# Kernel tuning notes

Hardware: AMD Instinct MI355X
Metric: run time of the kernel (lower is better)

Reference implementation:

```python
import jax, jax.numpy as jnp
import numpy as np

P = 7            # roi_align_size
S = 2            # sampling grid per bin (mmcv sampling_ratio fixed to 2 for static shapes)
CAV = (-140.8, -40.0, -3.0, 140.8, 40.0, 1.0)
ENLARGE = 1.0

def _bilinear(fmap, b, x, y):
    # fmap: [B,H,W,C]; b,x,y: [N,P,P,S,S]; returns [N,P,P,S,S,C]
    H, W = fmap.shape[1], fmap.shape[2]
    valid = (y > -1.0) & (y < H) & (x > -1.0) & (x < W)
    y = jnp.maximum(y, 0.0)
    x = jnp.maximum(x, 0.0)
    y0 = jnp.minimum(jnp.floor(y).astype(jnp.int32), H - 1)
    x0 = jnp.minimum(jnp.floor(x).astype(jnp.int32), W - 1)
    y1 = jnp.minimum(y0 + 1, H - 1)
    x1 = jnp.minimum(x0 + 1, W - 1)
    # mmcv: if low index is at the border, snap the coordinate onto it
    yf = jnp.where(y0 >= H - 1, y0.astype(y.dtype), y)
    xf = jnp.where(x0 >= W - 1, x0.astype(x.dtype), x)
    ly = yf - y0.astype(y.dtype); lx = xf - x0.astype(x.dtype)
    hy = 1.0 - ly; hx = 1.0 - lx
    v00 = fmap[b, y0, x0]; v01 = fmap[b, y0, x1]
    v10 = fmap[b, y1, x0]; v11 = fmap[b, y1, x1]
    out = ((hy * hx)[..., None] * v00 + (hy * lx)[..., None] * v01
           + (ly * hx)[..., None] * v10 + (ly * lx)[..., None] * v11)
    return out * valid.astype(out.dtype)[..., None]

def _forward(feature, boxes, mask):
    B, C, H, W = feature.shape
    M = boxes.shape[1]
    gw = (CAV[3] - CAV[0]) / W
    gh = (CAV[4] - CAV[1]) / H
    flat = boxes.reshape(B * M, 7)  # mask is all ones -> every box is a roi
    b_idx = jnp.repeat(jnp.arange(B, dtype=jnp.int32), M)
    # roi in grid coords; spatial_scale=1, aligned=True (center offset -0.5)
    cx = (flat[:, 0] - CAV[0]) / gw - 0.5
    cy = (flat[:, 1] - CAV[1]) / gh - 0.5
    rw = flat[:, 5] / gw * ENLARGE
    rh = flat[:, 4] / gh * ENLARGE
    theta = -flat[:, 6]             # clockwise=True -> negate angle
    bin_w = rw / P; bin_h = rh / P
    pw = jnp.arange(P, dtype=feature.dtype)
    sw = (jnp.arange(S, dtype=feature.dtype) + 0.5) / S
    # per-roi local sample coords: [N,P,S]
    xx = (-rw / 2.0)[:, None, None] + bin_w[:, None, None] * (pw[None, :, None] + sw[None, None, :])
    yy = (-rh / 2.0)[:, None, None] + bin_h[:, None, None] * (pw[None, :, None] + sw[None, None, :])
    cosv = jnp.cos(theta)[:, None, None, None, None]
    sinv = jnp.sin(theta)[:, None, None, None, None]
    Y = yy[:, :, None, :, None]     # [N,ph,1,iy,1]
    X = xx[:, None, :, None, :]     # [N,1,pw,1,ix]
    ys = Y * cosv - X * sinv + cy[:, None, None, None, None]
    xs = Y * sinv + X * cosv + cx[:, None, None, None, None]
    fmap = jnp.transpose(feature, (0, 2, 3, 1))   # [B,H,W,C] for channel-last gathers
    b = jnp.broadcast_to(b_idx[:, None, None, None, None], ys.shape)
    vals = _bilinear(fmap, b, xs, ys)             # [N,P,P,S,S,C]
    pooled = vals.mean(axis=(3, 4))               # [N,P,P,C] == torch .permute(0,2,3,1)
    return pooled

def setup_inputs():
    key = jax.random.key(0)
    k1, k2 = jax.random.split(key, 2)
    B, C, H, W, M = 4, 256, 256, 256, 100
    feature = jax.random.normal(k1, (B, C, H, W), jnp.float32)
    u = jax.random.uniform(k2, (B, M, 7), jnp.float32)
    boxes = jnp.stack([
        u[..., 0] * 200.0 - 100.0,       # x center in [-100,100] m
        u[..., 1] * 60.0 - 30.0,         # y center in [-30,30] m
        u[..., 2] * 2.0 - 1.0,           # z (unused)
        u[..., 3] * 2.0 + 1.0,           # dim (unused)
        u[..., 4] * 2.0 + 1.5,           # extent mapped to H axis
        u[..., 5] * 3.0 + 2.0,           # extent mapped to W axis
        u[..., 6] * 2.0 * np.pi - np.pi, # yaw
    ], axis=-1)
    mask = jnp.ones((B, M), jnp.float32)
    return {"feature": feature, "object_bbx_center": boxes, "object_bbx_mask": mask}

def reference(feature, object_bbx_center, object_bbx_mask):
    return _forward(feature, object_bbx_center, object_bbx_mask)
```

## Files before the change

kernel.cpp:

```cpp
#include <hip/hip_runtime.h>


#define RP 7
#define RS 2
#define RGN 16
#define CG 32
#define CSTRIDE (RGN * RGN + 1)
#define NSAMP (RP * RP * RS * RS)

__global__ __launch_bounds__(256) void roialign_kernel(
    const float* __restrict__ feature,
    const float* __restrict__ boxes,
    float* __restrict__ out,
    int C, int H, int W, int M)
{
    __shared__ float  sm[CG * CSTRIDE];
    __shared__ int4   soff[NSAMP];
    __shared__ float4 swt[NSAMP];
    __shared__ int    srowmax;

    const int g = blockIdx.x;
    const int n = blockIdx.y;
    const int t = threadIdx.x;
    const int b = n / M;

    const float gw = 281.6f / (float)W;
    const float gh = 80.0f  / (float)H;

    const float* bx = boxes + n * 7;
    const float cx = (bx[0] + 140.8f) / gw - 0.5f;
    const float cy = (bx[1] + 40.0f)  / gh - 0.5f;
    const float rw = bx[5] / gw;
    const float rh = bx[4] / gh;
    const float theta = -bx[6];
    const float ct = cosf(theta), st = sinf(theta);
    const float bw = rw / (float)RP, bh = rh / (float)RP;

    const float ex = 0.5f * (fabsf(rw * ct) + fabsf(rh * st));
    const float ey = 0.5f * (fabsf(rw * st) + fabsf(rh * ct));
    const int rx0 = min(max(0, (int)floorf(cx - ex)), W - 1);
    const int ry0 = min(max(0, (int)floorf(cy - ey)), H - 1);

    if (t == 0) srowmax = 0;
    __syncthreads();

    const float Hf = (float)H, Wf = (float)W;
    if (t < NSAMP) {
        const int bin = t >> 2;
        const int v = (t >> 1) & 1;
        const int u = t & 1;
        const int j = bin / RP;
        const int i = bin - j * RP;
        const float yy = -rh * 0.5f + bh * ((float)j + ((float)v + 0.5f) / (float)RS);
        const float xx = -rw * 0.5f + bw * ((float)i + ((float)u + 0.5f) / (float)RS);
        float y = yy * ct - xx * st + cy;
        float x = yy * st + xx * ct + cx;
        const bool valid = (y > -1.0f) & (y < Hf) & (x > -1.0f) & (x < Wf);
        y = fmaxf(y, 0.0f);
        x = fmaxf(x, 0.0f);
        const int y0 = min((int)floorf(y), H - 1);
        const int x0 = min((int)floorf(x), W - 1);
        const int y1 = min(y0 + 1, H - 1);
        const int x1 = min(x0 + 1, W - 1);
        const float ly = (y0 >= H - 1) ? 0.0f : (y - (float)y0);
        const float lx = (x0 >= W - 1) ? 0.0f : (x - (float)x0);
        const float hy = 1.0f - ly;
        const float hx = 1.0f - lx;
        const int ly0 = min(max(y0 - ry0, 0), RGN - 1);
        const int lx0 = min(max(x0 - rx0, 0), RGN - 1);
        const int ly1 = min(max(y1 - ry0, 0), RGN - 1);
        const int lx1 = min(max(x1 - rx0, 0), RGN - 1);
        int4 o;
        o.x = valid ? (ly0 * RGN + lx0) : 0;
        o.y = valid ? (ly0 * RGN + lx1) : 0;
        o.z = valid ? (ly1 * RGN + lx0) : 0;
        o.w = valid ? (ly1 * RGN + lx1) : 0;
        float4 w;
        w.x = valid ? (hy * hx) : 0.0f;
        w.y = valid ? (hy * lx) : 0.0f;
        w.z = valid ? (ly * hx) : 0.0f;
        w.w = valid ? (ly * lx) : 0.0f;
        soff[t] = o;
        swt[t]  = w;
        atomicMax(&srowmax, valid ? ly1 : 0);
    }
    __syncthreads();

    const int ny = srowmax + 1;
    const int sx = t & (RGN - 1);
    const int sy = t >> 4;
    const size_t planeHW = (size_t)H * W;
    if (sy < ny) {
        const int xg = min(rx0 + sx, W - 1);
        const int yg = min(ry0 + sy, H - 1);
        const float* fbase = feature + (size_t)(b * C + g * CG) * planeHW
                                     + (size_t)yg * W + xg;
        #pragma unroll
        for (int cs = 0; cs < CG; ++cs) {
            sm[cs * CSTRIDE + sy * RGN + sx] = fbase[(size_t)cs * planeHW];
        }
    }
    __syncthreads();

    const int c = t & (CG - 1);
    const int slice = t >> 5;
    const float* __restrict__ smc = sm + c * CSTRIDE;
    float* __restrict__ outn = out + ((size_t)n * (RP * RP)) * C + g * CG + c;

    for (int bidx = slice; bidx < RP * RP; bidx += 8) {
        float acc = 0.0f;
        #pragma unroll
        for (int sub = 0; sub < RS * RS; ++sub) {
            const int4   o = soff[bidx * 4 + sub];
            const float4 w = swt[bidx * 4 + sub];
            acc += w.x * smc[o.x] + w.y * smc[o.y]
                 + w.z * smc[o.z] + w.w * smc[o.w];
        }
        outn[(size_t)bidx * C] = acc * (1.0f / (RS * RS));
    }
}

extern "C" void kernel_launch(void* const* d_in, const int* in_sizes, int n_in,
                              void* d_out, int out_size, void* d_ws, size_t ws_size,
                              hipStream_t stream) {
    const float* feature = (const float*)d_in[0];
    const float* boxes   = (const float*)d_in[1];
    float* out = (float*)d_out;

    const int C = 256, H = 256, W = 256;
    const int N = in_sizes[1] / 7;
    const int B = in_sizes[0] / (C * H * W);
    const int M = N / B;

    dim3 grid(C / CG, N);
    dim3 block(256);
    roialign_kernel<<<grid, block, 0, stream>>>(feature, boxes, out, C, H, W, M);
}
```

Measured before the change: 335.7 us.

## Use 17x17 region tile with single base offset and 16-channel groups

Changes the staged feature region from a 16x16 grid to 17x17 and stores only one base offset per sample, deriving the four bilinear neighbours as o, o+1, o+RGW, o+RGW+1. Halves the channel group to 16, which doubles the number of blocks and gives more bins processed in parallel per block. The load loop is flattened so each thread copies up to two pixels per channel, covering only the rows actually needed. This trades fewer shared-memory offset loads and more parallelism for more blocks recomputing sample coordinates, and it changes border clamping semantics slightly.

Result: slower. 361.2 us (+7.6%).

```diff
diff --git a/kernel.cpp b/kernel.cpp
--- a/kernel.cpp
+++ b/kernel.cpp
@@ -3,9 +3,10 @@
 
 #define RP 7
 #define RS 2
-#define RGN 16
-#define CG 32
-#define CSTRIDE (RGN * RGN + 1)
+#define RGW 17
+#define RGH 17
+#define CG 16
+#define CPIX (RGW * RGH)
 #define NSAMP (RP * RP * RS * RS)
 
 __global__ __launch_bounds__(256) void roialign_kernel(
@@ -14,9 +15,9 @@
     float* __restrict__ out,
     int C, int H, int W, int M)
 {
-    __shared__ float  sm[CG * CSTRIDE];
-    __shared__ int4   soff[NSAMP];
+    __shared__ float  sm[CG * CPIX];
     __shared__ float4 swt[NSAMP];
+    __shared__ int    soff[NSAMP];
     __shared__ int    srowmax;
 
     const int g = blockIdx.x;
@@ -60,61 +61,52 @@
         x = fmaxf(x, 0.0f);
         const int y0 = min((int)floorf(y), H - 1);
         const int x0 = min((int)floorf(x), W - 1);
-        const int y1 = min(y0 + 1, H - 1);
-        const int x1 = min(x0 + 1, W - 1);
         const float ly = (y0 >= H - 1) ? 0.0f : (y - (float)y0);
         const float lx = (x0 >= W - 1) ? 0.0f : (x - (float)x0);
         const float hy = 1.0f - ly;
         const float hx = 1.0f - lx;
-        const int ly0 = min(max(y0 - ry0, 0), RGN - 1);
-        const int lx0 = min(max(x0 - rx0, 0), RGN - 1);
-        const int ly1 = min(max(y1 - ry0, 0), RGN - 1);
-        const int lx1 = min(max(x1 - rx0, 0), RGN - 1);
-        int4 o;
-        o.x = valid ? (ly0 * RGN + lx0) : 0;
-        o.y = valid ? (ly0 * RGN + lx1) : 0;
-        o.z = valid ? (ly1 * RGN + lx0) : 0;
-        o.w = valid ? (ly1 * RGN + lx1) : 0;
+        const int ly0 = min(max(y0 - ry0, 0), RGH - 2);
+        const int lx0 = min(max(x0 - rx0, 0), RGW - 2);
+        soff[t] = valid ? (ly0 * RGW + lx0) : 0;
         float4 w;
         w.x = valid ? (hy * hx) : 0.0f;
         w.y = valid ? (hy * lx) : 0.0f;
         w.z = valid ? (ly * hx) : 0.0f;
         w.w = valid ? (ly * lx) : 0.0f;
-        soff[t] = o;
-        swt[t]  = w;
-        atomicMax(&srowmax, valid ? ly1 : 0);
+        swt[t] = w;
+        atomicMax(&srowmax, valid ? ly0 : 0);
     }
     __syncthreads();
 
-    const int ny = srowmax + 1;
-    const int sx = t & (RGN - 1);
-    const int sy = t >> 4;
+    const int npix = (srowmax + 2) * RGW;
+    const int y0p = t / RGW,        x0p = t - y0p * RGW;
+    const int y1p = (t + 256) / RGW, x1p = (t + 256) - y1p * RGW;
     const size_t planeHW = (size_t)H * W;
-    if (sy < ny) {
-        const int xg = min(rx0 + sx, W - 1);
-        const int yg = min(ry0 + sy, H - 1);
-        const float* fbase = feature + (size_t)(b * C + g * CG) * planeHW
-                                     + (size_t)yg * W + xg;
-        #pragma unroll
-        for (int cs = 0; cs < CG; ++cs) {
-            sm[cs * CSTRIDE + sy * RGN + sx] = fbase[(size_t)cs * planeHW];
-        }
+    const float* fplane = feature + (size_t)(b * C + g * CG) * planeHW;
+    const int g0 = min(ry0 + y0p, H - 1) * W + min(rx0 + x0p, W - 1);
+    const int g1 = min(ry0 + y1p, H - 1) * W + min(rx0 + x1p, W - 1);
+    const bool p0 = (t < npix), p1 = (t + 256 < npix);
+    #pragma unroll
+    for (int cs = 0; cs < CG; ++cs) {
+        const float* pl = fplane + (size_t)cs * planeHW;
+        if (p0) sm[cs * CPIX + t]       = pl[g0];
+        if (p1) sm[cs * CPIX + t + 256] = pl[g1];
     }
     __syncthreads();
 
     const int c = t & (CG - 1);
-    const int slice = t >> 5;
-    const float* __restrict__ smc = sm + c * CSTRIDE;
+    const int slice = t >> 4;
+    const float* __restrict__ smc = sm + c * CPIX;
     float* __restrict__ outn = out + ((size_t)n * (RP * RP)) * C + g * CG + c;
 
-    for (int bidx = slice; bidx < RP * RP; bidx += 8) {
+    for (int bidx = slice; bidx < RP * RP; bidx += 16) {
         float acc = 0.0f;
         #pragma unroll
         for (int sub = 0; sub < RS * RS; ++sub) {
-            const int4   o = soff[bidx * 4 + sub];
+            const int    o = soff[bidx * 4 + sub];
             const float4 w = swt[bidx * 4 + sub];
-            acc += w.x * smc[o.x] + w.y * smc[o.y]
-                 + w.z * smc[o.z] + w.w * smc[o.w];
+            acc += w.x * smc[o]       + w.y * smc[o + 1]
+                 + w.z * smc[o + RGW] + w.w * smc[o + RGW + 1];
         }
         outn[(size_t)bidx * C] = acc * (1.0f / (RS * RS));
     }
```
